# Kernel tuning notes

Hardware: AMD Instinct MI355X
Metric: run time of the kernel (lower is better)

## Reference

```python
import jax, jax.numpy as jnp
import numpy as np

B, L, D, H = 4, 2048, 1024, 16
DH = D // H  # 64
MASK_VALUE = -1000000.0
EPS = 1e-12


def setup_inputs() -> dict:
    key = jax.random.key(0)
    ks = jax.random.split(key, 7)
    s = 1.0 / np.sqrt(D)
    x = jax.random.normal(ks[0], (B, L, D), dtype=jnp.float32)
    Wq = jax.random.uniform(ks[1], (D, H * DH), jnp.float32, -s, s)
    Wk = jax.random.uniform(ks[2], (D, H * DH), jnp.float32, -s, s)
    Wv = jax.random.uniform(ks[3], (D, H * DH), jnp.float32, -s, s)
    Wo = jax.random.uniform(ks[4], (H * DH, D), jnp.float32, -s, s)
    gamma = jnp.ones((D,), jnp.float32)
    beta = jnp.zeros((D,), jnp.float32)
    # causal mask: True positions are masked (query m cannot attend to key n > m)
    attn_mask = jnp.triu(jnp.ones((L, L), dtype=bool), k=1)
    return {"x": x, "Wq": Wq, "Wk": Wk, "Wv": Wv, "Wo": Wo,
            "gamma": gamma, "beta": beta, "attn_mask": attn_mask}


def _layernorm(y, gamma, beta):
    mu = jnp.mean(y, axis=-1, keepdims=True)
    var = jnp.mean(jnp.square(y - mu), axis=-1, keepdims=True)
    return (y - mu) * jax.lax.rsqrt(var + EPS) * gamma + beta


def reference(x, Wq, Wk, Wv, Wo, gamma, beta, attn_mask):
    scale = 1.0 / np.sqrt(DH)
    # projections, reshape to heads: B L (H D) -> B H L D
    q = (x @ Wq).reshape(B, L, H, DH).transpose(0, 2, 1, 3)
    k = (x @ Wk).reshape(B, L, H, DH).transpose(0, 2, 1, 3)
    v = (x @ Wv).reshape(B, L, H, DH).transpose(0, 2, 1, 3)
    scores = jnp.einsum('bhmd,bhnd->bhmn', q, k) * scale
    scores = jnp.where(attn_mask, MASK_VALUE, scores)
    probs = jax.nn.softmax(scores, axis=-1)
    z = jnp.einsum('bhmn,bhnd->bhmd', probs, v)
    z = z.transpose(0, 2, 1, 3).reshape(B, L, H * DH)
    out = jax.nn.relu(z @ Wo)
    return _layernorm(out + x, gamma, beta)
```

## Files before the change

### kernel.cpp

```cpp
#include <hip/hip_runtime.h>
#include <math.h>

#define B_ 4
#define L_ 2048
#define D_ 1024
#define H_ 16
#define DH_ 64
#define QKV_N 3072

typedef unsigned short ushort_t;
typedef unsigned int uint_t;
using bf16x8 = __attribute__((ext_vector_type(8))) short;
using f32x4  = __attribute__((ext_vector_type(4))) float;

__device__ __forceinline__ ushort_t f2bf(float f) {
    union { float f; unsigned int u; } v; v.f = f;
    unsigned int u = v.u;
    unsigned int rnd = ((u >> 16) & 1u) + 0x7fffu;
    return (ushort_t)((u + rnd) >> 16);
}

__device__ __forceinline__ float bf2f(ushort_t u) {
    union { unsigned int u; float f; } v;
    v.u = ((unsigned int)u) << 16;
    return v.f;
}

__device__ __forceinline__ void glds16(const void* g, void* l) {
    __builtin_amdgcn_global_load_lds(
        (const __attribute__((address_space(1))) unsigned int*)g,
        (__attribute__((address_space(3))) unsigned int*)l, 16, 0, 0);
}

__global__ __launch_bounds__(256) void prep(const float* __restrict__ Wq,
                                            const float* __restrict__ Wk,
                                            const float* __restrict__ Wv,
                                            const float* __restrict__ Wo,
                                            const float* __restrict__ x,
                                            ushort_t* __restrict__ wcat,
                                            ushort_t* __restrict__ wto,
                                            ushort_t* __restrict__ xb) {
    const int t = threadIdx.x;
    if (blockIdx.z == 4) {
        const int bid = blockIdx.y * 16 + blockIdx.x;
        const int base = bid * 32768 + t * 4;
        #pragma unroll
        for (int it = 0; it < 32; ++it) {
            float4 v = *(const float4*)(x + base + it * 1024);
            ushort4 o;
            o.x = f2bf(v.x); o.y = f2bf(v.y); o.z = f2bf(v.z); o.w = f2bf(v.w);
            *(ushort4*)(xb + base + it * 1024) = o;
        }
        return;
    }
    __shared__ ushort_t tile[64][65];
    const int widx = blockIdx.z;
    const float* W = (widx == 0) ? Wq : (widx == 1) ? Wk : (widx == 2) ? Wv : Wo;
    ushort_t* dst = (widx < 3) ? (wcat + (size_t)widx * 1024 * 1024) : wto;
    const int j = t & 63, i0 = t >> 6;
    const int kbase = blockIdx.y * 64, nbase = blockIdx.x * 64;
    #pragma unroll
    for (int it = 0; it < 16; ++it) {
        int i = it * 4 + i0;
        tile[i][j] = f2bf(W[(size_t)(kbase + i) * 1024 + nbase + j]);
    }
    __syncthreads();
    #pragma unroll
    for (int it = 0; it < 16; ++it) {
        int nn = it * 4 + i0;
        dst[(size_t)(nbase + nn) * 1024 + kbase + j] = tile[j][nn];
    }
}

__global__ __launch_bounds__(256) void gemm_mfma(const ushort_t* __restrict__ A,
                                                 const ushort_t* __restrict__ Wt,
                                                 ushort_t* __restrict__ Cbf,
                                                 const ushort_t* __restrict__ resid,
                                                 ushort_t* __restrict__ vt,
                                                 int M, int N, int K, int fuse) {
    __shared__ ushort_t As[128 * 64];
    __shared__ ushort_t Bs[128 * 64];
    const int t = threadIdx.x;
    const int w = t >> 6, ln = t & 63;
    const int l15 = ln & 15, quad = ln >> 4;
    const int bm = blockIdx.y * 128, bn = blockIdx.x * 128;
    const int wm = (w & 1) * 64, wn = (w >> 1) * 64;

    const ushort_t* Ap[4];
    const ushort_t* Bp[4];
    #pragma unroll
    for (int j = 0; j < 4; ++j) {
        const int i = t + j * 256;
        const int r = i >> 3;
        const int qg = (i & 7) ^ (r & 7);
        Ap[j] = A  + (size_t)(bm + r) * K + qg * 8;
        Bp[j] = Wt + (size_t)(bn + r) * K + qg * 8;
    }

    f32x4 acc[4][4] = {};

    for (int k0 = 0; k0 < K; k0 += 64) {
        __syncthreads();
        #pragma unroll
        for (int j = 0; j < 4; ++j) {
            glds16(Ap[j] + k0, &As[(t + j * 256) * 8]);
            glds16(Bp[j] + k0, &Bs[(t + j * 256) * 8]);
        }
        __syncthreads();

        #pragma unroll
        for (int kw = 0; kw < 2; ++kw) {
            bf16x8 af[4], bfr[4];
            #pragma unroll
            for (int im = 0; im < 4; ++im) {
                int row = wm + im * 16 + l15;
                int phys = (kw * 4 + quad) ^ (row & 7);
                af[im] = *(const bf16x8*)&As[row * 64 + phys * 8];
            }
            #pragma unroll
            for (int in = 0; in < 4; ++in) {
                int row = wn + in * 16 + l15;
                int phys = (kw * 4 + quad) ^ (row & 7);
                bfr[in] = *(const bf16x8*)&Bs[row * 64 + phys * 8];
            }
            #pragma unroll
            for (int im = 0; im < 4; ++im)
                #pragma unroll
                for (int in = 0; in < 4; ++in)
                    acc[im][in] = __builtin_amdgcn_mfma_f32_16x16x32_bf16(
                        af[im], bfr[in], acc[im][in], 0, 0, 0);
        }
    }

    if (vt && bn >= 2048) {
        #pragma unroll
        for (int im = 0; im < 4; ++im) {
            #pragma unroll
            for (int in = 0; in < 4; ++in) {
                #pragma unroll
                for (int reg = 0; reg < 4; ++reg) {
                    int row = bm + wm + im * 16 + quad * 4 + reg;
                    int col = bn + wn + in * 16 + l15 - 2048;
                    int bb = row >> 11, tok = row & 2047;
                    int h = col >> 6, d = col & 63;
                    int tg = tok & 63;
                    int sc = (tg & 15) * 4 + (tg >> 4);
                    size_t addr = ((size_t)((bb * 16 + h) * 64 + d) << 11)
                                + (tok & ~63) + sc;
                    vt[addr] = f2bf(acc[im][in][reg]);
                }
            }
        }
    } else {
        #pragma unroll
        for (int im = 0; im < 4; ++im) {
            #pragma unroll
            for (int in = 0; in < 4; ++in) {
                #pragma unroll
                for (int reg = 0; reg < 4; ++reg) {
                    int row = bm + wm + im * 16 + quad * 4 + reg;
                    int col = bn + wn + in * 16 + l15;
                    size_t idx = (size_t)row * N + col;
                    float v = acc[im][in][reg];
                    if (fuse) v = fmaxf(v, 0.f) + bf2f(resid[idx]);
                    Cbf[idx] = f2bf(v);
                }
            }
        }
    }
}

__global__ __launch_bounds__(256) void attn_mfma(const ushort_t* __restrict__ qkv,
                                                 const ushort_t* __restrict__ Vt,
                                                 ushort_t* __restrict__ Zb) {
    __shared__ ushort_t Ks[128 * 64];
    __shared__ ushort_t Vs[64 * 128];
    __shared__ ushort_t Ps[4][32 * 72];
    const int t = threadIdx.x, w = t >> 6, ln = t & 63;
    const int l15 = ln & 15, quad = ln >> 4;
    const int bh = blockIdx.x;
    const int b = bh >> 4, h = bh & 15;
    const int Qt = 15 - blockIdx.y;

    bf16x8 ones;
    #pragma unroll
    for (int i = 0; i < 8; ++i) ones[i] = (short)0x3f80;

    int kkey[4], kq[4], vd[4], vcq[4];
    #pragma unroll
    for (int j = 0; j < 4; ++j) {
        int i = t + j * 256;
        kkey[j] = i >> 3;
        kq[j]   = (i & 7) ^ (kkey[j] & 7);
        vd[j]   = i >> 4;
        int cqp = i & 15;
        vcq[j]  = (cqp & 8) | ((cqp & 7) ^ (vd[j] & 7));
    }
    const ushort_t* Kgb = qkv + 1024 + (size_t)b * L_ * QKV_N + h * DH_;
    const ushort_t* Vgb = Vt + (size_t)((b * H_ + h) * DH_) * L_;

    bf16x8 qf[2][2];
    #pragma unroll
    for (int mt = 0; mt < 2; ++mt) {
        const ushort_t* qrow =
            qkv + (size_t)(b * L_ + Qt * 128 + w * 32 + mt * 16 + l15) * QKV_N + h * DH_;
        qf[mt][0] = *(const bf16x8*)(qrow + quad * 8);
        qf[mt][1] = *(const bf16x8*)(qrow + 32 + quad * 8);
    }

    f32x4 acc_o[2][4] = {};
    f32x4 l_acc[2] = {};

    const float c2 = 0.18033688f;

    for (int kt = 0; kt <= Qt; ++kt) {
        __syncthreads();
        #pragma unroll
        for (int j = 0; j < 4; ++j) {
            glds16(Kgb + (size_t)(kt * 128 + kkey[j]) * QKV_N + kq[j] * 8,
                   &Ks[(t + j * 256) * 8]);
            glds16(Vgb + (size_t)vd[j] * L_ + kt * 128 + vcq[j] * 8,
                   &Vs[(t + j * 256) * 8]);
        }
        __syncthreads();

        const bool masked = (kt == Qt);

        #pragma unroll
        for (int ph = 0; ph < 2; ++ph) {
            if (masked && ph && w < 2) continue;

            f32x4 acc_s[2][4] = {};
            #pragma unroll
            for (int in = 0; in < 4; ++in) {
                const int key = ph * 64 + in * 16 + l15;
                #pragma unroll
                for (int ks = 0; ks < 2; ++ks) {
                    int phys = (ks * 4 + quad) ^ (key & 7);
                    bf16x8 kf = *(const bf16x8*)&Ks[key * 64 + phys * 8];
                    acc_s[0][in] = __builtin_amdgcn_mfma_f32_16x16x32_bf16(
                        qf[0][ks], kf, acc_s[0][in], 0, 0, 0);
                    acc_s[1][in] = __builtin_amdgcn_mfma_f32_16x16x32_bf16(
                        qf[1][ks], kf, acc_s[1][in], 0, 0, 0);
                }
            }

            #pragma unroll
            for (int mt = 0; mt < 2; ++mt) {
                #pragma unroll
                for (int reg = 0; reg < 4; ++reg) {
                    const int row = mt * 16 + quad * 4 + reg;
                    float pv[4];
                    #pragma unroll
                    for (int in = 0; in < 4; ++in) {
                        float s2 = fmaf(acc_s[mt][in][reg], c2, -2.0f);
                        if (masked) {
                            int col = kt * 128 + ph * 64 + in * 16 + l15;
                            int qg  = Qt * 128 + w * 32 + row;
                            s2 = (col > qg) ? -100000.0f : s2;
                        }
                        pv[in] = __builtin_amdgcn_exp2f(s2);
                    }
                    uint_t u01 = __builtin_amdgcn_perm(
                        __float_as_uint(pv[1]), __float_as_uint(pv[0]), 0x07060302u);
                    uint_t u23 = __builtin_amdgcn_perm(
                        __float_as_uint(pv[3]), __float_as_uint(pv[2]), 0x07060302u);
                    uint2* dst = (uint2*)&Ps[w][row * 72 + l15 * 4];
                    *dst = make_uint2(u01, u23);
                }
            }

            #pragma unroll
            for (int ks = 0; ks < 2; ++ks) {
                bf16x8 pf0 = *(const bf16x8*)&Ps[w][(l15) * 72 + ks * 32 + quad * 8];
                bf16x8 pf1 = *(const bf16x8*)&Ps[w][(16 + l15) * 72 + ks * 32 + quad * 8];
                #pragma unroll
                for (int in = 0; in < 4; ++in) {
                    const int d = in * 16 + l15;
                    int physv = ph * 8 + (((ks * 4 + quad) ^ (d & 7)));
                    bf16x8 vf = *(const bf16x8*)&Vs[d * 128 + physv * 8];
                    acc_o[0][in] = __builtin_amdgcn_mfma_f32_16x16x32_bf16(
                        vf, pf0, acc_o[0][in], 0, 0, 0);
                    acc_o[1][in] = __builtin_amdgcn_mfma_f32_16x16x32_bf16(
                        vf, pf1, acc_o[1][in], 0, 0, 0);
                }
                l_acc[0] = __builtin_amdgcn_mfma_f32_16x16x32_bf16(ones, pf0, l_acc[0], 0, 0, 0);
                l_acc[1] = __builtin_amdgcn_mfma_f32_16x16x32_bf16(ones, pf1, l_acc[1], 0, 0, 0);
            }
        }
    }

    #pragma unroll
    for (int mt = 0; mt < 2; ++mt) {
        const float inv = 1.0f / l_acc[mt][0];
        const int row = b * L_ + Qt * 128 + w * 32 + mt * 16 + l15;
        #pragma unroll
        for (int in = 0; in < 4; ++in) {
            const int dbase = h * DH_ + in * 16 + quad * 4;
            f32x4 a = acc_o[mt][in];
            ushort4 o;
            o.x = f2bf(a[0] * inv); o.y = f2bf(a[1] * inv);
            o.z = f2bf(a[2] * inv); o.w = f2bf(a[3] * inv);
            *(ushort4*)(Zb + (size_t)row * D_ + dbase) = o;
        }
    }
}

__global__ __launch_bounds__(64) void ln_kernel(const ushort_t* __restrict__ Y,
                                                const float* __restrict__ gamma,
                                                const float* __restrict__ beta,
                                                float* __restrict__ out) {
    const int row = blockIdx.x;
    const int t = threadIdx.x;
    const ushort_t* y = Y + (size_t)row * D_;

    float v[16];
    #pragma unroll
    for (int s = 0; s < 4; ++s) {
        ushort4 u = *(const ushort4*)(y + s * 256 + t * 4);
        v[s * 4 + 0] = bf2f(u.x);
        v[s * 4 + 1] = bf2f(u.y);
        v[s * 4 + 2] = bf2f(u.z);
        v[s * 4 + 3] = bf2f(u.w);
    }

    float sum = 0.f;
    #pragma unroll
    for (int i = 0; i < 16; ++i) sum += v[i];
    #pragma unroll
    for (int k = 1; k < 64; k <<= 1) sum += __shfl_xor(sum, k, 64);
    const float mu = sum * (1.f / (float)D_);

    float var = 0.f;
    #pragma unroll
    for (int i = 0; i < 16; ++i) {
        float d = v[i] - mu;
        var += d * d;
    }
    #pragma unroll
    for (int k = 1; k < 64; k <<= 1) var += __shfl_xor(var, k, 64);
    const float rstd = rsqrtf(var * (1.f / (float)D_) + 1e-12f);

    #pragma unroll
    for (int s = 0; s < 4; ++s) {
        const int col = s * 256 + t * 4;
        float4 g  = *(const float4*)(gamma + col);
        float4 bb = *(const float4*)(beta + col);
        float4 o;
        o.x = (v[s * 4 + 0] - mu) * rstd * g.x + bb.x;
        o.y = (v[s * 4 + 1] - mu) * rstd * g.y + bb.y;
        o.z = (v[s * 4 + 2] - mu) * rstd * g.z + bb.z;
        o.w = (v[s * 4 + 3] - mu) * rstd * g.w + bb.w;
        *(float4*)(out + (size_t)row * D_ + col) = o;
    }
}

extern "C" void kernel_launch(void* const* d_in, const int* in_sizes, int n_in,
                              void* d_out, int out_size, void* d_ws, size_t ws_size,
                              hipStream_t stream) {
    const float* x     = (const float*)d_in[0];
    const float* Wq    = (const float*)d_in[1];
    const float* Wk    = (const float*)d_in[2];
    const float* Wv    = (const float*)d_in[3];
    const float* Wo    = (const float*)d_in[4];
    const float* gamma = (const float*)d_in[5];
    const float* beta  = (const float*)d_in[6];
    float* out = (float*)d_out;

    char* ws = (char*)d_ws;
    ushort_t* x_bf = (ushort_t*)(ws);
    ushort_t* wcat = (ushort_t*)(ws + (16u  << 20));
    ushort_t* wto  = (ushort_t*)(ws + (22u  << 20));
    ushort_t* qkv  = (ushort_t*)(ws + (24u  << 20));
    ushort_t* vt   = (ushort_t*)(ws + (72u  << 20));
    ushort_t* z_bf = (ushort_t*)(ws + (88u  << 20));
    ushort_t* y_bf = (ushort_t*)(ws + (104u << 20));

    const int M = B_ * L_;

    prep<<<dim3(16, 16, 5), 256, 0, stream>>>(Wq, Wk, Wv, Wo, x, wcat, wto, x_bf);

    gemm_mfma<<<dim3(QKV_N / 128, M / 128), 256, 0, stream>>>(
        x_bf, wcat, qkv, nullptr, vt, M, QKV_N, D_, 0);

    attn_mfma<<<dim3(B_ * H_, 16), 256, 0, stream>>>(qkv, vt, z_bf);

    gemm_mfma<<<dim3(D_ / 128, M / 128), 256, 0, stream>>>(
        z_bf, wto, y_bf, x_bf, nullptr, M, D_, D_, 1);

    ln_kernel<<<M, 64, 0, stream>>>(y_bf, gamma, beta, out);
}
```

Baseline: 283.2 us.

## Add 256x256-tile 8-wave GEMM with LDS pipelining for QKV projection

Adds a new GEMM kernel with 256x256 block tiles, 512 threads, and double-buffered direct global-to-LDS loads with swizzled layout. It uses phased barriers, setprio around the MFMA bursts, and an XCD-aware block remap. It replaces the 128x128 GEMM only for the QKV projection, aiming for more data reuse per tile and better overlap of loads with MFMA. The grid shrinks to 12x32=384 blocks, so occupancy per CU drops and the register pressure of 128 accumulator floats per thread rises.

New measurement: 278.3 us. About the same (-1.7%).

```diff
diff --git a/kernel.cpp b/kernel.cpp
--- a/kernel.cpp
+++ b/kernel.cpp
@@ -69,6 +69,152 @@
     for (int it = 0; it < 16; ++it) {
         int nn = it * 4 + i0;
         dst[(size_t)(nbase + nn) * 1024 + kbase + j] = tile[j][nn];
+    }
+}
+
+__global__ __launch_bounds__(512) void gemm256(const ushort_t* __restrict__ A,
+                                               const ushort_t* __restrict__ Wt,
+                                               ushort_t* __restrict__ Cbf,
+                                               const ushort_t* __restrict__ resid,
+                                               ushort_t* __restrict__ vt,
+                                               int M, int N, int K, int fuse) {
+    __shared__ ushort_t lds[2][2][2][8192];
+    const int t = threadIdx.x;
+    const int w = t >> 6, ln = t & 63;
+    const int l15 = ln & 15, quad = ln >> 4;
+    const int wrow = w >> 2, wcol = w & 3;
+
+    int bx = blockIdx.x, by = blockIdx.y;
+    {
+        int nwg = gridDim.x * gridDim.y;
+        if ((nwg & 7) == 0) {
+            int flat = by * gridDim.x + bx;
+            int nid = (flat & 7) * (nwg >> 3) + (flat >> 3);
+            by = nid / gridDim.x;
+            bx = nid - by * gridDim.x;
+        }
+    }
+    const int bm = by * 256, bn = bx * 256;
+
+    const ushort_t* Agp[2];
+    const ushort_t* Bgp[2];
+    #pragma unroll
+    for (int j = 0; j < 2; ++j) {
+        int r = j * 128 + (t >> 2);
+        int c = (t & 3) ^ ((r >> 1) & 3);
+        Agp[j] = A  + (size_t)(bm + r) * K + c * 8;
+        Bgp[j] = Wt + (size_t)(bn + r) * K + c * 8;
+    }
+
+    const int swz8 = (quad ^ ((l15 >> 1) & 3)) * 8;
+    int aoff[8], boff[4];
+    #pragma unroll
+    for (int mf = 0; mf < 8; ++mf)
+        aoff[mf] = (wrow * 128 + mf * 16 + l15) * 32 + swz8;
+    #pragma unroll
+    for (int nf = 0; nf < 4; ++nf)
+        boff[nf] = (wcol * 64 + nf * 16 + l15) * 32 + swz8;
+
+    f32x4 acc[8][4] = {};
+    bf16x8 bfq[4];
+    const int NT = K >> 6;
+
+#define STAGE(BUF, AB, KH, KT) do {                                         \
+        glds16(((AB) ? Bgp[0] : Agp[0]) + (KT) * 64 + (KH) * 32,            \
+               &lds[BUF][AB][KH][t * 8]);                                   \
+        glds16(((AB) ? Bgp[1] : Agp[1]) + (KT) * 64 + (KH) * 32,            \
+               &lds[BUF][AB][KH][4096 + t * 8]);                            \
+    } while (0)
+
+#define VM4 asm volatile("s_waitcnt vmcnt(4)" ::: "memory")
+#define VM0 asm volatile("s_waitcnt vmcnt(0)" ::: "memory")
+#define NOVM ((void)0)
+
+#define PHASE(BUF, KH, MH, LOADB, STAGEC, VMW) do {                         \
+        bf16x8 af_[4];                                                      \
+        _Pragma("unroll")                                                   \
+        for (int m_ = 0; m_ < 4; ++m_)                                      \
+            af_[m_] = *(const bf16x8*)&lds[BUF][0][KH][aoff[(MH) * 4 + m_]];\
+        if (LOADB) {                                                        \
+            _Pragma("unroll")                                               \
+            for (int n_ = 0; n_ < 4; ++n_)                                  \
+                bfq[n_] = *(const bf16x8*)&lds[BUF][1][KH][boff[n_]];       \
+        }                                                                   \
+        STAGEC;                                                             \
+        VMW;                                                                \
+        __builtin_amdgcn_s_barrier();                                       \
+        asm volatile("s_waitcnt lgkmcnt(0)" ::: "memory");                  \
+        __builtin_amdgcn_s_setprio(1);                                      \
+        _Pragma("unroll")                                                   \
+        for (int m_ = 0; m_ < 4; ++m_)                                      \
+            _Pragma("unroll")                                               \
+            for (int n_ = 0; n_ < 4; ++n_)                                  \
+                acc[(MH) * 4 + m_][n_] =                                    \
+                    __builtin_amdgcn_mfma_f32_16x16x32_bf16(                \
+                        af_[m_], bfq[n_], acc[(MH) * 4 + m_][n_], 0, 0, 0); \
+        __builtin_amdgcn_s_setprio(0);                                      \
+        __builtin_amdgcn_s_barrier();                                       \
+    } while (0)
+
+    STAGE(0, 0, 0, 0); STAGE(0, 1, 0, 0);
+    STAGE(0, 0, 1, 0); STAGE(0, 1, 1, 0);
+    STAGE(1, 0, 0, 1); STAGE(1, 1, 0, 1);
+    VM4;
+    __builtin_amdgcn_s_barrier();
+
+    for (int it = 0; it < (NT >> 1); ++it) {
+        const int kt1 = 2 * it + 1, kt2 = 2 * it + 2, kt3 = 2 * it + 3;
+        const bool g2 = kt2 < NT, g3 = kt3 < NT;
+        PHASE(0, 0, 0, 1, STAGE(1, 0, 1, kt1), NOVM);
+        PHASE(0, 0, 1, 0, STAGE(1, 1, 1, kt1), NOVM);
+        PHASE(0, 1, 0, 1, if (g2) STAGE(0, 0, 0, kt2), NOVM);
+        PHASE(0, 1, 1, 0, if (g2) STAGE(0, 1, 0, kt2),
+              { if (g2) { VM4; } else { VM0; } });
+        PHASE(1, 0, 0, 1, if (g2) STAGE(0, 0, 1, kt2), NOVM);
+        PHASE(1, 0, 1, 0, if (g2) STAGE(0, 1, 1, kt2), NOVM);
+        PHASE(1, 1, 0, 1, if (g3) STAGE(1, 0, 0, kt3), NOVM);
+        PHASE(1, 1, 1, 0, if (g3) STAGE(1, 1, 0, kt3),
+              { if (g3) { VM4; } else { VM0; } });
+    }
+
+#undef PHASE
+#undef STAGE
+
+    if (vt && bn >= 2048) {
+        #pragma unroll
+        for (int mf = 0; mf < 8; ++mf) {
+            #pragma unroll
+            for (int nf = 0; nf < 4; ++nf) {
+                #pragma unroll
+                for (int reg = 0; reg < 4; ++reg) {
+                    int row = bm + wrow * 128 + mf * 16 + quad * 4 + reg;
+                    int col = bn + wcol * 64 + nf * 16 + l15 - 2048;
+                    int bb = row >> 11, tok = row & 2047;
+                    int h = col >> 6, d = col & 63;
+                    int tg = tok & 63;
+                    int sc = (tg & 15) * 4 + (tg >> 4);
+                    size_t addr = ((size_t)((bb * 16 + h) * 64 + d) << 11)
+                                + (tok & ~63) + sc;
+                    vt[addr] = f2bf(acc[mf][nf][reg]);
+                }
+            }
+        }
+    } else {
+        #pragma unroll
+        for (int mf = 0; mf < 8; ++mf) {
+            #pragma unroll
+            for (int nf = 0; nf < 4; ++nf) {
+                #pragma unroll
+                for (int reg = 0; reg < 4; ++reg) {
+                    int row = bm + wrow * 128 + mf * 16 + quad * 4 + reg;
+                    int col = bn + wcol * 64 + nf * 16 + l15;
+                    size_t idx = (size_t)row * N + col;
+                    float v = acc[mf][nf][reg];
+                    if (fuse) v = fmaxf(v, 0.f) + bf2f(resid[idx]);
+                    Cbf[idx] = f2bf(v);
+                }
+            }
+        }
     }
 }
 
@@ -380,7 +526,7 @@
 
     prep<<<dim3(16, 16, 5), 256, 0, stream>>>(Wq, Wk, Wv, Wo, x, wcat, wto, x_bf);
 
-    gemm_mfma<<<dim3(QKV_N / 128, M / 128), 256, 0, stream>>>(
+    gemm256<<<dim3(QKV_N / 256, M / 256), 512, 0, stream>>>(
         x_bf, wcat, qkv, nullptr, vt, M, QKV_N, D_, 0);
 
     attn_mfma<<<dim3(B_ * H_, 16), 256, 0, stream>>>(qkv, vt, z_bf);
```
